# Performance work log

Hardware: AMD Instinct MI355X
Metric: run time of the kernel (lower is better)

## Reference

```python
import jax, jax.numpy as jnp
import numpy as np

B, L, D = 4096, 200, 64
N_ITEMS, N_USERS, N_RATINGS = 100000, 100000, 5


def setup_inputs() -> dict:
    key = jax.random.key(0)
    ks = jax.random.split(key, 10)
    nodes = jax.random.randint(ks[0], (B,), 0, N_USERS)
    history_uv = jax.random.randint(ks[1], (B, L), 0, N_ITEMS)
    history_r = jax.random.randint(ks[2], (B, L), 0, N_RATINGS)
    s = 1.0 / np.sqrt(D)
    v2e = jax.random.normal(ks[3], (N_ITEMS, D), dtype=jnp.float32)
    r2e = jax.random.normal(ks[4], (N_RATINGS, D), dtype=jnp.float32)
    # torch Linear: weight is [out, in]
    w1_W = jax.random.uniform(ks[5], (D, 2 * D), dtype=jnp.float32, minval=-s, maxval=s)
    w1_b = jax.random.uniform(ks[6], (D,), dtype=jnp.float32, minval=-s, maxval=s)
    w2_W = jax.random.uniform(ks[7], (D, D), dtype=jnp.float32, minval=-s, maxval=s)
    w2_b = jax.random.uniform(ks[8], (D,), dtype=jnp.float32, minval=-s, maxval=s)
    return {
        "v2e": v2e, "r2e": r2e,
        "w1_W": w1_W, "w1_b": w1_b, "w2_W": w2_W, "w2_b": w2_b,
        "nodes": nodes, "history_uv": history_uv, "history_r": history_r,
    }


def reference(v2e, r2e, w1_W, w1_b, w2_W, w2_b, nodes, history_uv, history_r):
    # Gather item and rating embeddings for every (node, history slot): [B, L, D]
    e_uv = v2e[history_uv]
    e_r = r2e[history_r]
    # concat -> [B, L, 2D], two-layer MLP with ReLU
    x = jnp.concatenate([e_uv, e_r], axis=-1)
    h = jax.nn.relu(jnp.einsum("bli,oi->blo", x, w1_W) + w1_b)
    o = jax.nn.relu(jnp.einsum("bli,oi->blo", h, w2_W) + w2_b)
    # uv=True branch: plain mean over the history dimension (nodes/u2e unused)
    return jnp.mean(o, axis=1)  # [B, D]
```

## Files before the change

kernel.cpp:

```cpp
#include <hip/hip_runtime.h>

#define NITEMS 100000
#define NRATE  5
#define BB     4096
#define LL     200
#define DD     64
#define NTILES 6250

typedef short short8  __attribute__((ext_vector_type(8)));
typedef float f32x4   __attribute__((ext_vector_type(4)));
typedef float f32x2   __attribute__((ext_vector_type(2)));
typedef int   i32x4   __attribute__((ext_vector_type(4)));

static __device__ __forceinline__ short f2bf(float f) {
  return (short)((__builtin_bit_cast(unsigned, f) + 0x8000u) >> 16);
}
static __device__ __forceinline__ unsigned pk2bf(float a, float b) {
  const unsigned ua = __builtin_bit_cast(unsigned, a) + 0x8000u;
  const unsigned ub = __builtin_bit_cast(unsigned, b) + 0x8000u;
  return __builtin_amdgcn_perm(ub, ua, 0x07060302u);
}
static __device__ __forceinline__ int kperm(int p) {
  return ((p & 3) << 4) | (p >> 2);
}

#if __has_builtin(__builtin_elementwise_max)
static __device__ __forceinline__ f32x2 relu2(f32x2 v) {
  return __builtin_elementwise_max(v, f32x2{0.f, 0.f});
}
static __device__ __forceinline__ f32x4 relu4(f32x4 v) {
  return __builtin_elementwise_max(v, f32x4{0.f, 0.f, 0.f, 0.f});
}
#else
static __device__ __forceinline__ f32x2 relu2(f32x2 v) {
  return f32x2{fmaxf(v.x, 0.f), fmaxf(v.y, 0.f)};
}
static __device__ __forceinline__ f32x4 relu4(f32x4 v) {
  return f32x4{fmaxf(v[0], 0.f), fmaxf(v[1], 0.f), fmaxf(v[2], 0.f), fmaxf(v[3], 0.f)};
}
#endif

__global__ __launch_bounds__(256) void k_pre(
    const float* __restrict__ v2e, const float* __restrict__ r2e,
    const float* __restrict__ w1W, const float* __restrict__ w1b,
    const float* __restrict__ w2W,
    unsigned char* __restrict__ pre8, short* __restrict__ w2p,
    float* __restrict__ r5p)
{
  const int tid = threadIdx.x;
  const int blk = blockIdx.x;

  if (blk == 0) {
    for (int idx = tid; idx < 64 * 64; idx += 256) {
      const int o = idx >> 6, p = idx & 63;
      w2p[idx] = f2bf(w2W[o * 64 + kperm(p)]);
    }
    for (int idx = tid; idx < NRATE * 64; idx += 256) {
      const int r = idx >> 6, p = idx & 63;
      const int o = kperm(p);
      const float4* wr = reinterpret_cast<const float4*>(w1W + o * 128 + 64);
      const float4* rr = reinterpret_cast<const float4*>(r2e + r * 64);
      float s = w1b[o];
#pragma unroll
      for (int q = 0; q < 16; ++q) {
        const float4 a = wr[q], b = rr[q];
        s += a.x * b.x + a.y * b.y + a.z * b.z + a.w * b.w;
      }
      r5p[r * 64 + p] = s;
    }
    return;
  }

  const int wave = tid >> 6, lane = tid & 63;
  const int n = lane & 15, quad = lane >> 4;
  const int tile = (blk - 1) * 4 + wave;
  if (tile >= NTILES) return;

  const int q0 = ((n >> 1) & 3) * 16 + (n >> 3) * 8 + (n & 1) * 4;

  const size_t row = (size_t)(tile * 16 + n);
  const float4* pv = reinterpret_cast<const float4*>(v2e + row * 64 + quad * 8);
  const float4* qv = reinterpret_cast<const float4*>(v2e + row * 64 + 32 + quad * 8);
  const float4 cur0 = pv[0], cur1 = pv[1], cur2 = qv[0], cur3 = qv[1];

  short8 bfr[2][4];
#pragma unroll
  for (int nt = 0; nt < 4; ++nt)
#pragma unroll
    for (int kh = 0; kh < 2; ++kh) {
      const float4* p = reinterpret_cast<const float4*>(
          w1W + (nt * 16 + n) * 128 + kh * 32 + quad * 8);
      const float4 x0 = p[0], x1 = p[1];
      i32x4 pk = {(int)pk2bf(x0.x, x0.y), (int)pk2bf(x0.z, x0.w),
                  (int)pk2bf(x1.x, x1.y), (int)pk2bf(x1.z, x1.w)};
      bfr[kh][nt] = __builtin_bit_cast(short8, pk);
    }

  short8 afr[2];
  {
    i32x4 pk0 = {(int)pk2bf(cur0.x, cur0.y), (int)pk2bf(cur0.z, cur0.w),
                 (int)pk2bf(cur1.x, cur1.y), (int)pk2bf(cur1.z, cur1.w)};
    afr[0] = __builtin_bit_cast(short8, pk0);
    i32x4 pk1 = {(int)pk2bf(cur2.x, cur2.y), (int)pk2bf(cur2.z, cur2.w),
                 (int)pk2bf(cur3.x, cur3.y), (int)pk2bf(cur3.z, cur3.w)};
    afr[1] = __builtin_bit_cast(short8, pk1);
  }

  f32x4 d[4];
#pragma unroll
  for (int nt = 0; nt < 4; ++nt) {
    f32x4 z = {0.f, 0.f, 0.f, 0.f};
    z = __builtin_amdgcn_mfma_f32_16x16x32_bf16(afr[0], bfr[0][nt], z, 0, 0, 0);
    z = __builtin_amdgcn_mfma_f32_16x16x32_bf16(afr[1], bfr[1][nt], z, 0, 0, 0);
    d[nt] = z;
  }

  const int ib = tile * 16;
#pragma unroll
  for (int r = 0; r < 4; ++r) {
    const int item = ib + quad * 4 + r;
    int pkd = 0;
    pkd = __builtin_amdgcn_cvt_pk_fp8_f32(d[0][r], d[1][r], pkd, false);
    pkd = __builtin_amdgcn_cvt_pk_fp8_f32(d[2][r], d[3][r], pkd, true);
    *reinterpret_cast<int*>(pre8 + (size_t)item * 64 + q0) = pkd;
  }
}

__global__ __launch_bounds__(256) void k_main(
    const unsigned char* __restrict__ pre8, const float* __restrict__ r5p,
    const short* __restrict__ w2p, const float* __restrict__ w2b,
    const int* __restrict__ huv, const int* __restrict__ hrr,
    float* __restrict__ out)
{
  __shared__ __align__(16) float s_r5[4][5 * 68];

  const int tid  = threadIdx.x;
  const int wave = tid >> 6, lane = tid & 63;
  const int n = lane & 15, quad = lane >> 4;
  const int b = blockIdx.x * 4 + wave;

  const int* hu = huv + b * LL;
  const int* hr = hrr + b * LL;

  int iv[13], ir[13];
#pragma unroll
  for (int t = 0; t < 12; ++t) {
    iv[t] = hu[t * 16 + n];
    ir[t] = hr[t * 16 + n];
  }
  {
    const int lc = min(192 + n, LL - 1);
    iv[12] = hu[lc];
    ir[12] = hr[lc];
  }

  i32x4 g[13];
#pragma unroll
  for (int t = 0; t < 13; ++t)
    g[t] = *reinterpret_cast<const i32x4*>(
        pre8 + (size_t)iv[t] * 64 + quad * 16);

#pragma unroll
  for (int i = 0; i < 5; ++i) {
    const int idx = i * 64 + lane;
    s_r5[wave][(idx >> 6) * 68 + (idx & 63)] = r5p[idx];
  }

  short8 bfr[2][4];
#pragma unroll
  for (int nt = 0; nt < 4; ++nt)
#pragma unroll
    for (int kh = 0; kh < 2; ++kh)
      bfr[kh][nt] = *reinterpret_cast<const short8*>(
          w2p + (nt * 16 + n) * 64 + kh * 32 + quad * 8);

  f32x4 zb[4];
#pragma unroll
  for (int nt = 0; nt < 4; ++nt) {
    const float bv = w2b[nt * 16 + n];
    zb[nt] = f32x4{bv, bv, bv, bv};
  }

  const float tailm = (quad < 2) ? 1.0f : 0.0f;
  f32x4 acc4[4] = {{0.f,0.f,0.f,0.f},{0.f,0.f,0.f,0.f},
                   {0.f,0.f,0.f,0.f},{0.f,0.f,0.f,0.f}};

#pragma unroll
  for (int t = 0; t < 13; ++t) {
    const float* rbase = &s_r5[wave][ir[t] * 68 + quad * 8];
    short8 afr[2];
    {
      const f32x2* rp = reinterpret_cast<const f32x2*>(rbase);
      f32x2 p0 = relu2(__builtin_amdgcn_cvt_pk_f32_fp8(g[t][0], false) + rp[0]);
      f32x2 p1 = relu2(__builtin_amdgcn_cvt_pk_f32_fp8(g[t][0], true)  + rp[1]);
      f32x2 p2 = relu2(__builtin_amdgcn_cvt_pk_f32_fp8(g[t][1], false) + rp[2]);
      f32x2 p3 = relu2(__builtin_amdgcn_cvt_pk_f32_fp8(g[t][1], true)  + rp[3]);
      i32x4 hpk = {(int)pk2bf(p0.x, p0.y), (int)pk2bf(p1.x, p1.y),
                   (int)pk2bf(p2.x, p2.y), (int)pk2bf(p3.x, p3.y)};
      afr[0] = __builtin_bit_cast(short8, hpk);
    }
    {
      const f32x2* rp = reinterpret_cast<const f32x2*>(rbase + 32);
      f32x2 p0 = relu2(__builtin_amdgcn_cvt_pk_f32_fp8(g[t][2], false) + rp[0]);
      f32x2 p1 = relu2(__builtin_amdgcn_cvt_pk_f32_fp8(g[t][2], true)  + rp[1]);
      f32x2 p2 = relu2(__builtin_amdgcn_cvt_pk_f32_fp8(g[t][3], false) + rp[2]);
      f32x2 p3 = relu2(__builtin_amdgcn_cvt_pk_f32_fp8(g[t][3], true)  + rp[3]);
      i32x4 hpk = {(int)pk2bf(p0.x, p0.y), (int)pk2bf(p1.x, p1.y),
                   (int)pk2bf(p2.x, p2.y), (int)pk2bf(p3.x, p3.y)};
      afr[1] = __builtin_bit_cast(short8, hpk);
    }

    f32x4 d[4];
#pragma unroll
    for (int nt = 0; nt < 4; ++nt) {
      f32x4 z = zb[nt];
      z = __builtin_amdgcn_mfma_f32_16x16x32_bf16(afr[0], bfr[0][nt], z, 0, 0, 0);
      z = __builtin_amdgcn_mfma_f32_16x16x32_bf16(afr[1], bfr[1][nt], z, 0, 0, 0);
      d[nt] = z;
    }

#pragma unroll
    for (int nt = 0; nt < 4; ++nt) {
      f32x4 mx = relu4(d[nt]);
      if (t == 12) mx = mx * tailm;
      acc4[nt] += mx;
    }
  }

  float acc[4];
#pragma unroll
  for (int nt = 0; nt < 4; ++nt) {
    float v = (acc4[nt][0] + acc4[nt][1]) + (acc4[nt][2] + acc4[nt][3]);
    v += __shfl_xor(v, 16, 64);
    v += __shfl_xor(v, 32, 64);
    acc[nt] = v;
  }

  out[b * 64 + quad * 16 + n] = acc[quad] * (1.0f / (float)LL);
}

__global__ __launch_bounds__(256) void k_fallback(
    const float* __restrict__ v2e, const float* __restrict__ r2e,
    const float* __restrict__ w1W, const float* __restrict__ w1b,
    const float* __restrict__ w2W, const float* __restrict__ w2b,
    const int* __restrict__ huv, const int* __restrict__ hrr,
    float* __restrict__ out)
{
  __shared__ float sw1[64][129];
  __shared__ float sw2[64][65];
  __shared__ float sx[4][128];
  __shared__ float sh[4][64];
  __shared__ float red[4][64];

  const int tid = threadIdx.x;
  const int wave = tid >> 6, lane = tid & 63;
  const int b = blockIdx.x;

  for (int idx = tid; idx < 64 * 128; idx += 256) sw1[idx >> 7][idx & 127] = w1W[idx];
  for (int idx = tid; idx < 64 * 64; idx += 256) sw2[idx >> 6][idx & 63] = w2W[idx];
  __syncthreads();

  const float b1o = w1b[lane], b2o = w2b[lane];
  float acc = 0.f;

  for (int l = wave; l < LL; l += 4) {
    const int iv = huv[b * LL + l];
    const int ir = hrr[b * LL + l];
    sx[wave][lane]      = v2e[iv * 64 + lane];
    sx[wave][64 + lane] = r2e[ir * 64 + lane];
    __syncthreads();
    float h = b1o;
    for (int i = 0; i < 128; ++i) h += sx[wave][i] * sw1[lane][i];
    sh[wave][lane] = fmaxf(h, 0.f);
    __syncthreads();
    float o = b2o;
    for (int i = 0; i < 64; ++i) o += sh[wave][i] * sw2[lane][i];
    acc += fmaxf(o, 0.f);
  }

  red[wave][lane] = acc;
  __syncthreads();
  if (tid < 64) {
    const float s = red[0][tid] + red[1][tid] + red[2][tid] + red[3][tid];
    out[b * 64 + tid] = s * (1.0f / (float)LL);
  }
}

extern "C" void kernel_launch(void* const* d_in, const int* in_sizes, int n_in,
                              void* d_out, int out_size, void* d_ws, size_t ws_size,
                              hipStream_t stream) {
  (void)in_sizes; (void)n_in; (void)out_size;
  const float* v2e = (const float*)d_in[0];
  const float* r2e = (const float*)d_in[1];
  const float* w1W = (const float*)d_in[2];
  const float* w1b = (const float*)d_in[3];
  const float* w2W = (const float*)d_in[4];
  const float* w2b = (const float*)d_in[5];
  const int* huv = (const int*)d_in[7];
  const int* hrr = (const int*)d_in[8];
  float* out = (float*)d_out;

  const size_t OFF_R5 = (size_t)NITEMS * 64;
  const size_t OFF_W2 = OFF_R5 + NRATE * 64 * sizeof(float);
  const size_t NEED   = OFF_W2 + 64 * 64 * sizeof(short);

  if (ws_size >= NEED) {
    unsigned char* pre8 = (unsigned char*)d_ws;
    float* r5p = (float*)((char*)d_ws + OFF_R5);
    short* w2p = (short*)((char*)d_ws + OFF_W2);

    k_pre<<<1564, 256, 0, stream>>>(v2e, r2e, w1W, w1b, w2W, pre8, w2p, r5p);
    k_main<<<BB / 4, 256, 0, stream>>>(pre8, r5p, w2p, w2b, huv, hrr, out);
  } else {
    k_fallback<<<BB, 256, 0, stream>>>(v2e, r2e, w1W, w1b, w2W, w2b, huv, hrr, out);
  }
}
```

Before: 117.0 us.

## Process two tiles per wave in k_pre with prefetch; vectorize LDS reads and set MFMA priority

The precompute kernel now launches half as many blocks. Each wave handles up to two item tiles with a stride of NWAVES, loading the next tile's v2e rows while the current one is converted and run through MFMA. This amortises the per-wave W1 fragment loading and hides global load latency. In k_main, the per-rating bias reads from LDS are widened from float2 to float4 loads, and s_setprio raises wave priority around the MFMA block. The risks are higher register pressure and fewer resident waves in k_pre.

After: 114.1 us, median of 2. -2.5%, faster.

```diff
diff --git a/kernel.cpp b/kernel.cpp
--- a/kernel.cpp
+++ b/kernel.cpp
@@ -6,6 +6,8 @@
 #define LL     200
 #define DD     64
 #define NTILES 6250
+#define NWAVES 3128
+#define NW_REM 3122
 
 typedef short short8  __attribute__((ext_vector_type(8)));
 typedef float f32x4   __attribute__((ext_vector_type(4)));
@@ -73,15 +75,20 @@
 
   const int wave = tid >> 6, lane = tid & 63;
   const int n = lane & 15, quad = lane >> 4;
-  const int tile = (blk - 1) * 4 + wave;
-  if (tile >= NTILES) return;
+  const int gw = (blk - 1) * 4 + wave;
+  const int ntile = (gw < NW_REM) ? 2 : 1;
 
   const int q0 = ((n >> 1) & 3) * 16 + (n >> 3) * 8 + (n & 1) * 4;
 
-  const size_t row = (size_t)(tile * 16 + n);
-  const float4* pv = reinterpret_cast<const float4*>(v2e + row * 64 + quad * 8);
-  const float4* qv = reinterpret_cast<const float4*>(v2e + row * 64 + 32 + quad * 8);
-  const float4 cur0 = pv[0], cur1 = pv[1], cur2 = qv[0], cur3 = qv[1];
+  int tile = gw;
+  float4 cur0, cur1, cur2, cur3;
+  {
+    const size_t row = (size_t)(tile * 16 + n);
+    const float4* p = reinterpret_cast<const float4*>(v2e + row * 64 + quad * 8);
+    cur0 = p[0]; cur1 = p[1];
+    const float4* q = reinterpret_cast<const float4*>(v2e + row * 64 + 32 + quad * 8);
+    cur2 = q[0]; cur3 = q[1];
+  }
 
   short8 bfr[2][4];
 #pragma unroll
@@ -96,33 +103,48 @@
       bfr[kh][nt] = __builtin_bit_cast(short8, pk);
     }
 
-  short8 afr[2];
-  {
-    i32x4 pk0 = {(int)pk2bf(cur0.x, cur0.y), (int)pk2bf(cur0.z, cur0.w),
-                 (int)pk2bf(cur1.x, cur1.y), (int)pk2bf(cur1.z, cur1.w)};
-    afr[0] = __builtin_bit_cast(short8, pk0);
-    i32x4 pk1 = {(int)pk2bf(cur2.x, cur2.y), (int)pk2bf(cur2.z, cur2.w),
-                 (int)pk2bf(cur3.x, cur3.y), (int)pk2bf(cur3.z, cur3.w)};
-    afr[1] = __builtin_bit_cast(short8, pk1);
-  }
-
-  f32x4 d[4];
-#pragma unroll
-  for (int nt = 0; nt < 4; ++nt) {
-    f32x4 z = {0.f, 0.f, 0.f, 0.f};
-    z = __builtin_amdgcn_mfma_f32_16x16x32_bf16(afr[0], bfr[0][nt], z, 0, 0, 0);
-    z = __builtin_amdgcn_mfma_f32_16x16x32_bf16(afr[1], bfr[1][nt], z, 0, 0, 0);
-    d[nt] = z;
-  }
-
-  const int ib = tile * 16;
-#pragma unroll
-  for (int r = 0; r < 4; ++r) {
-    const int item = ib + quad * 4 + r;
-    int pkd = 0;
-    pkd = __builtin_amdgcn_cvt_pk_fp8_f32(d[0][r], d[1][r], pkd, false);
-    pkd = __builtin_amdgcn_cvt_pk_fp8_f32(d[2][r], d[3][r], pkd, true);
-    *reinterpret_cast<int*>(pre8 + (size_t)item * 64 + q0) = pkd;
+  for (int it = 0; it < ntile; ++it) {
+    const int next = tile + NWAVES;
+    float4 nx0, nx1, nx2, nx3;
+    if (it + 1 < ntile) {
+      const size_t row = (size_t)(next * 16 + n);
+      const float4* p = reinterpret_cast<const float4*>(v2e + row * 64 + quad * 8);
+      nx0 = p[0]; nx1 = p[1];
+      const float4* q = reinterpret_cast<const float4*>(v2e + row * 64 + 32 + quad * 8);
+      nx2 = q[0]; nx3 = q[1];
+    }
+
+    short8 afr[2];
+    {
+      i32x4 pk0 = {(int)pk2bf(cur0.x, cur0.y), (int)pk2bf(cur0.z, cur0.w),
+                   (int)pk2bf(cur1.x, cur1.y), (int)pk2bf(cur1.z, cur1.w)};
+      afr[0] = __builtin_bit_cast(short8, pk0);
+      i32x4 pk1 = {(int)pk2bf(cur2.x, cur2.y), (int)pk2bf(cur2.z, cur2.w),
+                   (int)pk2bf(cur3.x, cur3.y), (int)pk2bf(cur3.z, cur3.w)};
+      afr[1] = __builtin_bit_cast(short8, pk1);
+    }
+
+    f32x4 d[4];
+#pragma unroll
+    for (int nt = 0; nt < 4; ++nt) {
+      f32x4 z = {0.f, 0.f, 0.f, 0.f};
+      z = __builtin_amdgcn_mfma_f32_16x16x32_bf16(afr[0], bfr[0][nt], z, 0, 0, 0);
+      z = __builtin_amdgcn_mfma_f32_16x16x32_bf16(afr[1], bfr[1][nt], z, 0, 0, 0);
+      d[nt] = z;
+    }
+
+    const int ib = tile * 16;
+#pragma unroll
+    for (int r = 0; r < 4; ++r) {
+      const int item = ib + quad * 4 + r;
+      int pkd = 0;
+      pkd = __builtin_amdgcn_cvt_pk_fp8_f32(d[0][r], d[1][r], pkd, false);
+      pkd = __builtin_amdgcn_cvt_pk_fp8_f32(d[2][r], d[3][r], pkd, true);
+      *reinterpret_cast<int*>(pre8 + (size_t)item * 64 + q0) = pkd;
+    }
+
+    tile = next;
+    cur0 = nx0; cur1 = nx1; cur2 = nx2; cur3 = nx3;
   }
 }
 
@@ -188,28 +210,32 @@
 #pragma unroll
   for (int t = 0; t < 13; ++t) {
     const float* rbase = &s_r5[wave][ir[t] * 68 + quad * 8];
+    const f32x4 ra = *reinterpret_cast<const f32x4*>(rbase);
+    const f32x4 rb = *reinterpret_cast<const f32x4*>(rbase + 4);
+    const f32x4 rc = *reinterpret_cast<const f32x4*>(rbase + 32);
+    const f32x4 rd = *reinterpret_cast<const f32x4*>(rbase + 36);
+
     short8 afr[2];
     {
-      const f32x2* rp = reinterpret_cast<const f32x2*>(rbase);
-      f32x2 p0 = relu2(__builtin_amdgcn_cvt_pk_f32_fp8(g[t][0], false) + rp[0]);
-      f32x2 p1 = relu2(__builtin_amdgcn_cvt_pk_f32_fp8(g[t][0], true)  + rp[1]);
-      f32x2 p2 = relu2(__builtin_amdgcn_cvt_pk_f32_fp8(g[t][1], false) + rp[2]);
-      f32x2 p3 = relu2(__builtin_amdgcn_cvt_pk_f32_fp8(g[t][1], true)  + rp[3]);
+      f32x2 p0 = relu2(__builtin_amdgcn_cvt_pk_f32_fp8(g[t][0], false) + f32x2{ra[0], ra[1]});
+      f32x2 p1 = relu2(__builtin_amdgcn_cvt_pk_f32_fp8(g[t][0], true)  + f32x2{ra[2], ra[3]});
+      f32x2 p2 = relu2(__builtin_amdgcn_cvt_pk_f32_fp8(g[t][1], false) + f32x2{rb[0], rb[1]});
+      f32x2 p3 = relu2(__builtin_amdgcn_cvt_pk_f32_fp8(g[t][1], true)  + f32x2{rb[2], rb[3]});
       i32x4 hpk = {(int)pk2bf(p0.x, p0.y), (int)pk2bf(p1.x, p1.y),
                    (int)pk2bf(p2.x, p2.y), (int)pk2bf(p3.x, p3.y)};
       afr[0] = __builtin_bit_cast(short8, hpk);
     }
     {
-      const f32x2* rp = reinterpret_cast<const f32x2*>(rbase + 32);
-      f32x2 p0 = relu2(__builtin_amdgcn_cvt_pk_f32_fp8(g[t][2], false) + rp[0]);
-      f32x2 p1 = relu2(__builtin_amdgcn_cvt_pk_f32_fp8(g[t][2], true)  + rp[1]);
-      f32x2 p2 = relu2(__builtin_amdgcn_cvt_pk_f32_fp8(g[t][3], false) + rp[2]);
-      f32x2 p3 = relu2(__builtin_amdgcn_cvt_pk_f32_fp8(g[t][3], true)  + rp[3]);
+      f32x2 p0 = relu2(__builtin_amdgcn_cvt_pk_f32_fp8(g[t][2], false) + f32x2{rc[0], rc[1]});
+      f32x2 p1 = relu2(__builtin_amdgcn_cvt_pk_f32_fp8(g[t][2], true)  + f32x2{rc[2], rc[3]});
+      f32x2 p2 = relu2(__builtin_amdgcn_cvt_pk_f32_fp8(g[t][3], false) + f32x2{rd[0], rd[1]});
+      f32x2 p3 = relu2(__builtin_amdgcn_cvt_pk_f32_fp8(g[t][3], true)  + f32x2{rd[2], rd[3]});
       i32x4 hpk = {(int)pk2bf(p0.x, p0.y), (int)pk2bf(p1.x, p1.y),
                    (int)pk2bf(p2.x, p2.y), (int)pk2bf(p3.x, p3.y)};
       afr[1] = __builtin_bit_cast(short8, hpk);
     }
 
+    __builtin_amdgcn_s_setprio(1);
     f32x4 d[4];
 #pragma unroll
     for (int nt = 0; nt < 4; ++nt) {
@@ -218,6 +244,7 @@
       z = __builtin_amdgcn_mfma_f32_16x16x32_bf16(afr[1], bfr[1][nt], z, 0, 0, 0);
       d[nt] = z;
     }
+    __builtin_amdgcn_s_setprio(0);
 
 #pragma unroll
     for (int nt = 0; nt < 4; ++nt) {
@@ -309,7 +336,7 @@
     float* r5p = (float*)((char*)d_ws + OFF_R5);
     short* w2p = (short*)((char*)d_ws + OFF_W2);
 
-    k_pre<<<1564, 256, 0, stream>>>(v2e, r2e, w1W, w1b, w2W, pre8, w2p, r5p);
+    k_pre<<<783, 256, 0, stream>>>(v2e, r2e, w1W, w1b, w2W, pre8, w2p, r5p);
     k_main<<<BB / 4, 256, 0, stream>>>(pre8, r5p, w2p, w2b, huv, hrr, out);
   } else {
     k_fallback<<<BB, 256, 0, stream>>>(v2e, r2e, w1W, w1b, w2W, w2b, huv, hrr, out);
```
